# Optimization experiments

Measured on AMD Instinct MI355X. Metric: run time of the kernel, lower is better.

Reference implementation:

```python
import jax, jax.numpy as jnp
import numpy as np

PI = 3.141592653  # same constant as the torch source
M = 4
MIN_LAMBDA = 5.0
MAX_LAMBDA = 1500.0
IT = 1  # first forward call


def setup_inputs() -> dict:
    key = jax.random.key(0)
    k1, k2, k3 = jax.random.split(key, 3)
    N, D, C = 512, 512, 100000
    x = jax.random.normal(k1, (N, D), dtype=jnp.float32)
    target = jax.random.randint(k2, (N,), 0, C, dtype=jnp.int64)
    weight = jax.random.normal(k3, (D, C), dtype=jnp.float32)
    return {"x": x, "target": target, "weight": weight}


def reference(x, target, weight):
    # normalize weight columns (dim=0), as in F.normalize(w, p=2, dim=0)
    w = weight / jnp.linalg.norm(weight, axis=0, keepdims=True)
    w_norm = jnp.linalg.norm(w, axis=0, keepdims=True)          # [1, C] (~1)
    x_norm = jnp.linalg.norm(x, axis=1, keepdims=True)          # [N, 1]

    cos_theta = x @ w                                           # [N, C]
    cos_theta = jnp.clip(cos_theta / x_norm / w_norm, -1.0, 1.0)

    rows = jnp.arange(x.shape[0])
    c_t = cos_theta[rows, target]                               # [N]
    # m=4 multi-angle: cos(4t) = 8c^4 - 8c^2 + 1
    cos_m_theta = 8.0 * c_t ** 4 - 8.0 * c_t ** 2 + 1.0
    theta = jnp.arccos(c_t)
    k = jnp.floor(M * theta / PI)
    sign = 1.0 - 2.0 * (k % 2.0)                                # (-1)^k for integer-valued float k
    phi_t = sign * cos_m_theta - 2.0 * k

    cur_lambda = max(MIN_LAMBDA, MAX_LAMBDA / (1.0 + 0.1 * IT))
    addition = (phi_t - c_t) * x_norm[:, 0] / (1.0 + cur_lambda)

    out = cos_theta * x_norm                                    # [N, C]
    out = out.at[rows, target].add(addition)
    return out
```

## Files before the change

### kernel.cpp

```cpp
#include <hip/hip_runtime.h>
#include <hip/hip_bf16.h>

typedef __attribute__((ext_vector_type(4))) float f32x4;
typedef __attribute__((ext_vector_type(8))) short s16x8;

#define NR 512
#define KD 512
#define CC 100000
#define BN 32
#define LDSK 40

static __device__ __forceinline__ unsigned short f2bf(float f) {
    union { float f; unsigned u; } v; v.f = f;
    unsigned r = v.u + 0x7FFFu + ((v.u >> 16) & 1u);
    return (unsigned short)(r >> 16);
}

__global__ __launch_bounds__(256) void prep_kernel(const float* __restrict__ x,
                                                   float* __restrict__ xn,
                                                   unsigned short* __restrict__ xb) {
    const int row = blockIdx.x;
    const int t = threadIdx.x;
    const float* xr = x + row * KD;
    float v0 = xr[t];
    float v1 = xr[t + 256];
    float ss = v0 * v0 + v1 * v1;
    #pragma unroll
    for (int off = 32; off > 0; off >>= 1) ss += __shfl_down(ss, off, 64);
    __shared__ float sred[4];
    if ((t & 63) == 0) sred[t >> 6] = ss;
    __syncthreads();
    if (t == 0) xn[row] = sqrtf(sred[0] + sred[1] + sred[2] + sred[3]);
    xb[row * KD + t]       = f2bf(v0);
    xb[row * KD + t + 256] = f2bf(v1);
}

__global__ __launch_bounds__(256, 3) void gemm_kernel(const float* __restrict__ w,
                                                      const unsigned short* __restrict__ xb,
                                                      const float* __restrict__ xn,
                                                      float* __restrict__ out) {
    __shared__ unsigned short ldsB[BN * LDSK];
    __shared__ float sPart[8][BN];
    __shared__ float sInv[BN];

    const int t    = threadIdx.x;
    const int lane = t & 63;
    const int wv   = t >> 6;
    const int c0   = blockIdx.x * BN;
    const int cL   = t & 31;
    const int kq   = t >> 5;

    f32x4 acc[8][2];
    #pragma unroll
    for (int i = 0; i < 8; ++i) {
        acc[i][0] = {0.f, 0.f, 0.f, 0.f};
        acc[i][1] = {0.f, 0.f, 0.f, 0.f};
    }

    float ss = 0.0f;
    const int rowbase = wv * 128;
    const int arow = lane & 15;
    const int akq  = lane >> 4;

    const float* wp0 = w + (size_t)(kq * 4) * CC + c0 + cL;
    float bc0 = wp0[0];
    float bc1 = wp0[(size_t)CC];
    float bc2 = wp0[(size_t)2 * CC];
    float bc3 = wp0[(size_t)3 * CC];

    const unsigned short* abase = xb + (rowbase + arow) * KD + akq * 8;

    #pragma unroll 1
    for (int it = 0; it < 16; ++it) {
        const int kk = it * 32;

        s16x8 af[8];
        #pragma unroll
        for (int rt = 0; rt < 8; ++rt)
            af[rt] = *(const s16x8*)(abase + rt * 16 * KD + kk);

        float bn0 = 0.f, bn1 = 0.f, bn2 = 0.f, bn3 = 0.f;
        if (it < 15) {
            const float* wp = w + (size_t)(kk + 32 + kq * 4) * CC + c0 + cL;
            bn0 = wp[0];
            bn1 = wp[(size_t)CC];
            bn2 = wp[(size_t)2 * CC];
            bn3 = wp[(size_t)3 * CC];
        }

        ss += bc0 * bc0 + bc1 * bc1 + bc2 * bc2 + bc3 * bc3;
        ushort4 pk;
        pk.x = f2bf(bc0);
        pk.y = f2bf(bc1);
        pk.z = f2bf(bc2);
        pk.w = f2bf(bc3);

        __syncthreads();
        *(ushort4*)&ldsB[cL * LDSK + kq * 4] = pk;
        __syncthreads();

        const s16x8 bf0 = *(const s16x8*)&ldsB[(0 * 16 + arow) * LDSK + akq * 8];
        const s16x8 bf1 = *(const s16x8*)&ldsB[(1 * 16 + arow) * LDSK + akq * 8];

        #pragma unroll
        for (int rt = 0; rt < 8; ++rt) {
            acc[rt][0] = __builtin_amdgcn_mfma_f32_16x16x32_bf16(af[rt], bf0, acc[rt][0], 0, 0, 0);
            acc[rt][1] = __builtin_amdgcn_mfma_f32_16x16x32_bf16(af[rt], bf1, acc[rt][1], 0, 0, 0);
        }
        bc0 = bn0; bc1 = bn1; bc2 = bn2; bc3 = bn3;
    }

    sPart[kq][cL] = ss;
    __syncthreads();
    if (t < BN) {
        float tot = 0.f;
        #pragma unroll
        for (int i = 0; i < 8; ++i) tot += sPart[i][t];
        sInv[t] = 1.0f / sqrtf(tot);
    }
    __syncthreads();

    #pragma unroll
    for (int rt = 0; rt < 8; ++rt) {
        const int rbase = rowbase + rt * 16 + akq * 4;
        const f32x4 xnv = *(const f32x4*)(xn + rbase);
        #pragma unroll
        for (int ct = 0; ct < 2; ++ct) {
            const float inv = sInv[ct * 16 + arow];
            float* op = out + (size_t)rbase * CC + c0 + ct * 16 + arow;
            #pragma unroll
            for (int r = 0; r < 4; ++r) {
                float cv = acc[rt][ct][r] * inv / xnv[r];
                cv = fminf(1.0f, fmaxf(-1.0f, cv));
                op[(size_t)r * CC] = cv * xnv[r];
            }
        }
    }
}

__global__ __launch_bounds__(512) void fixup_kernel(const int* __restrict__ target,
                                                    const float* __restrict__ xn,
                                                    float* __restrict__ out) {
    const int i = threadIdx.x;
    const int tg = target[i];
    const float xni = xn[i];
    float* p = out + (size_t)i * CC + tg;
    const float val = *p;
    float c = val / xni;
    c = fminf(1.0f, fmaxf(-1.0f, c));
    const float c2 = c * c;
    const float cosm = 8.0f * c2 * c2 - 8.0f * c2 + 1.0f;
    const float theta = acosf(c);
    const float kf = floorf(4.0f * theta / 3.141592653f);
    const float sign = (((int)kf) & 1) ? -1.0f : 1.0f;
    const float phi = sign * cosm - 2.0f * kf;
    const float lam = 1500.0f / 1.1f;
    const float add = (phi - c) * xni / (1.0f + lam);
    *p = val + add;
}

extern "C" void kernel_launch(void* const* d_in, const int* in_sizes, int n_in,
                              void* d_out, int out_size, void* d_ws, size_t ws_size,
                              hipStream_t stream) {
    const float* x      = (const float*)d_in[0];
    const int*   target = (const int*)d_in[1];
    const float* w      = (const float*)d_in[2];
    float* out = (float*)d_out;

    float* xn = (float*)d_ws;
    unsigned short* xb = (unsigned short*)((char*)d_ws + 2048);

    prep_kernel<<<NR, 256, 0, stream>>>(x, xn, xb);
    gemm_kernel<<<CC / BN, 256, 0, stream>>>(w, xb, xn, out);
    fixup_kernel<<<1, 512, 0, stream>>>(target, xn, out);
}
```

Baseline: 522.0 us.

## Restructure GEMM tile to 64 columns with double-buffered LDS and deep weight prefetch

Widens the column tile to 64 and splits the rows across two blocks per column group, so each wave computes a 64x64 output tile. Weight loads are prefetched four stages ahead in registers, and the bf16 tile is double-buffered in LDS so each stage needs one barrier instead of two. It also raises MFMA priority, simplifies the clamp to avoid a divide, and writes the output with nontemporal stores. The cost is that each weight column is read by two blocks and each thread holds more live registers, which can lower occupancy.

Measured after the change: 566.7 us. 8.6% more time.

```diff
diff --git a/kernel.cpp b/kernel.cpp
--- a/kernel.cpp
+++ b/kernel.cpp
@@ -1,5 +1,4 @@
 #include <hip/hip_runtime.h>
-#include <hip/hip_bf16.h>
 
 typedef __attribute__((ext_vector_type(4))) float f32x4;
 typedef __attribute__((ext_vector_type(8))) short s16x8;
@@ -7,8 +6,9 @@
 #define NR 512
 #define KD 512
 #define CC 100000
-#define BN 32
+#define BN 64
 #define LDSK 40
+#define NSTG 16
 
 static __device__ __forceinline__ unsigned short f2bf(float f) {
     union { float f; unsigned u; } v; v.f = f;
@@ -35,104 +35,142 @@
     xb[row * KD + t + 256] = f2bf(v1);
 }
 
+#define CONVERT_STAGE(BUF, S)                                                        \
+  do {                                                                               \
+    ss += S[0]*S[0] + S[1]*S[1] + S[2]*S[2] + S[3]*S[3]                              \
+        + S[4]*S[4] + S[5]*S[5] + S[6]*S[6] + S[7]*S[7];                             \
+    ushort4 p0_, p1_;                                                                \
+    p0_.x = f2bf(S[0]); p0_.y = f2bf(S[1]); p0_.z = f2bf(S[2]); p0_.w = f2bf(S[3]);  \
+    p1_.x = f2bf(S[4]); p1_.y = f2bf(S[5]); p1_.z = f2bf(S[6]); p1_.w = f2bf(S[7]);  \
+    *(ushort4*)&ldsB[BUF][cL * LDSK + kg * 8]     = p0_;                             \
+    *(ushort4*)&ldsB[BUF][cL * LDSK + kg * 8 + 4] = p1_;                             \
+  } while (0)
+
 __global__ __launch_bounds__(256, 3) void gemm_kernel(const float* __restrict__ w,
                                                       const unsigned short* __restrict__ xb,
                                                       const float* __restrict__ xn,
                                                       float* __restrict__ out) {
-    __shared__ unsigned short ldsB[BN * LDSK];
-    __shared__ float sPart[8][BN];
+    __shared__ __align__(16) unsigned short ldsB[2][BN * LDSK];
+    __shared__ float sPart[4][BN];
     __shared__ float sInv[BN];
 
     const int t    = threadIdx.x;
     const int lane = t & 63;
     const int wv   = t >> 6;
-    const int c0   = blockIdx.x * BN;
-    const int cL   = t & 31;
-    const int kq   = t >> 5;
-
-    f32x4 acc[8][2];
-    #pragma unroll
-    for (int i = 0; i < 8; ++i) {
-        acc[i][0] = {0.f, 0.f, 0.f, 0.f};
-        acc[i][1] = {0.f, 0.f, 0.f, 0.f};
-    }
-
-    float ss = 0.0f;
-    const int rowbase = wv * 128;
+    const int ci   = blockIdx.x >> 1;
+    const int half = blockIdx.x & 1;
+    const int c0   = ci * BN;
+
+    const int cL = lane;
+    const int kg = wv;
+    int cg = c0 + cL;
+    if (cg > CC - 1) cg = CC - 1;
+    const float* wcol = w + cg;
+
+    const int rowbase = half * 256 + wv * 64;
     const int arow = lane & 15;
     const int akq  = lane >> 4;
-
-    const float* wp0 = w + (size_t)(kq * 4) * CC + c0 + cL;
-    float bc0 = wp0[0];
-    float bc1 = wp0[(size_t)CC];
-    float bc2 = wp0[(size_t)2 * CC];
-    float bc3 = wp0[(size_t)3 * CC];
-
-    const unsigned short* abase = xb + (rowbase + arow) * KD + akq * 8;
-
-    #pragma unroll 1
-    for (int it = 0; it < 16; ++it) {
-        const int kk = it * 32;
-
-        s16x8 af[8];
-        #pragma unroll
-        for (int rt = 0; rt < 8; ++rt)
-            af[rt] = *(const s16x8*)(abase + rt * 16 * KD + kk);
-
-        float bn0 = 0.f, bn1 = 0.f, bn2 = 0.f, bn3 = 0.f;
-        if (it < 15) {
-            const float* wp = w + (size_t)(kk + 32 + kq * 4) * CC + c0 + cL;
-            bn0 = wp[0];
-            bn1 = wp[(size_t)CC];
-            bn2 = wp[(size_t)2 * CC];
-            bn3 = wp[(size_t)3 * CC];
-        }
-
-        ss += bc0 * bc0 + bc1 * bc1 + bc2 * bc2 + bc3 * bc3;
-        ushort4 pk;
-        pk.x = f2bf(bc0);
-        pk.y = f2bf(bc1);
-        pk.z = f2bf(bc2);
-        pk.w = f2bf(bc3);
-
-        __syncthreads();
-        *(ushort4*)&ldsB[cL * LDSK + kq * 4] = pk;
-        __syncthreads();
-
-        const s16x8 bf0 = *(const s16x8*)&ldsB[(0 * 16 + arow) * LDSK + akq * 8];
-        const s16x8 bf1 = *(const s16x8*)&ldsB[(1 * 16 + arow) * LDSK + akq * 8];
-
-        #pragma unroll
-        for (int rt = 0; rt < 8; ++rt) {
-            acc[rt][0] = __builtin_amdgcn_mfma_f32_16x16x32_bf16(af[rt], bf0, acc[rt][0], 0, 0, 0);
-            acc[rt][1] = __builtin_amdgcn_mfma_f32_16x16x32_bf16(af[rt], bf1, acc[rt][1], 0, 0, 0);
-        }
-        bc0 = bn0; bc1 = bn1; bc2 = bn2; bc3 = bn3;
+    const unsigned short* abase = xb + (size_t)(rowbase + arow) * KD + akq * 8;
+
+    f32x4 acc[4][4];
+    #pragma unroll
+    for (int i = 0; i < 4; ++i)
+        #pragma unroll
+        for (int j = 0; j < 4; ++j)
+            acc[i][j] = {0.f, 0.f, 0.f, 0.f};
+
+    float ss = 0.f;
+
+    float s0[8], b0[8], b1[8], b2[8];
+    #pragma unroll
+    for (int r = 0; r < 8; ++r) s0[r] = wcol[(size_t)(kg * 8 + r) * CC];
+    s16x8 af[4];
+    #pragma unroll
+    for (int rt = 0; rt < 4; ++rt) af[rt] = *(const s16x8*)(abase + rt * 16 * KD);
+    #pragma unroll
+    for (int r = 0; r < 8; ++r) b0[r] = wcol[(size_t)(32 + kg * 8 + r) * CC];
+    #pragma unroll
+    for (int r = 0; r < 8; ++r) b1[r] = wcol[(size_t)(64 + kg * 8 + r) * CC];
+    #pragma unroll
+    for (int r = 0; r < 8; ++r) b2[r] = wcol[(size_t)(96 + kg * 8 + r) * CC];
+
+    CONVERT_STAGE(0, s0);
+    asm volatile("s_waitcnt lgkmcnt(0)" ::: "memory");
+    __builtin_amdgcn_s_barrier();
+
+    #pragma unroll
+    for (int i = 0; i < NSTG; ++i) {
+        s16x8 bf[4];
+        #pragma unroll
+        for (int ct = 0; ct < 4; ++ct)
+            bf[ct] = *(const s16x8*)&ldsB[i & 1][(ct * 16 + arow) * LDSK + akq * 8];
+
+        float bn[8];
+        if (i + 4 < NSTG) {
+            #pragma unroll
+            for (int r = 0; r < 8; ++r)
+                bn[r] = wcol[(size_t)((i + 4) * 32 + kg * 8 + r) * CC];
+        } else {
+            #pragma unroll
+            for (int r = 0; r < 8; ++r) bn[r] = 0.f;
+        }
+
+        s16x8 afn[4];
+        if (i + 1 < NSTG) {
+            #pragma unroll
+            for (int rt = 0; rt < 4; ++rt)
+                afn[rt] = *(const s16x8*)(abase + rt * 16 * KD + (i + 1) * 32);
+        } else {
+            #pragma unroll
+            for (int rt = 0; rt < 4; ++rt) afn[rt] = af[rt];
+        }
+
+        if (i + 1 < NSTG) {
+            CONVERT_STAGE((i + 1) & 1, b0);
+        }
+
+        asm volatile("s_waitcnt lgkmcnt(0)" ::: "memory");
+        __builtin_amdgcn_s_barrier();
+
+        __builtin_amdgcn_s_setprio(1);
+        #pragma unroll
+        for (int rt = 0; rt < 4; ++rt)
+            #pragma unroll
+            for (int ct = 0; ct < 4; ++ct)
+                acc[rt][ct] = __builtin_amdgcn_mfma_f32_16x16x32_bf16(af[rt], bf[ct], acc[rt][ct], 0, 0, 0);
+        __builtin_amdgcn_s_setprio(0);
+
+        #pragma unroll
+        for (int r = 0; r < 8; ++r) { b0[r] = b1[r]; b1[r] = b2[r]; b2[r] = bn[r]; }
+        #pragma unroll
+        for (int rt = 0; rt < 4; ++rt) af[rt] = afn[rt];
     }
 
-    sPart[kq][cL] = ss;
+    sPart[kg][cL] = ss;
     __syncthreads();
     if (t < BN) {
-        float tot = 0.f;
-        #pragma unroll
-        for (int i = 0; i < 8; ++i) tot += sPart[i][t];
+        const float tot = sPart[0][t] + sPart[1][t] + sPart[2][t] + sPart[3][t];
         sInv[t] = 1.0f / sqrtf(tot);
     }
     __syncthreads();
 
     #pragma unroll
-    for (int rt = 0; rt < 8; ++rt) {
+    for (int rt = 0; rt < 4; ++rt) {
         const int rbase = rowbase + rt * 16 + akq * 4;
         const f32x4 xnv = *(const f32x4*)(xn + rbase);
         #pragma unroll
-        for (int ct = 0; ct < 2; ++ct) {
-            const float inv = sInv[ct * 16 + arow];
-            float* op = out + (size_t)rbase * CC + c0 + ct * 16 + arow;
-            #pragma unroll
-            for (int r = 0; r < 4; ++r) {
-                float cv = acc[rt][ct][r] * inv / xnv[r];
-                cv = fminf(1.0f, fmaxf(-1.0f, cv));
-                op[(size_t)r * CC] = cv * xnv[r];
+        for (int ct = 0; ct < 4; ++ct) {
+            const int col = c0 + ct * 16 + arow;
+            if (col < CC) {
+                const float inv = sInv[ct * 16 + arow];
+                float* op = out + (size_t)rbase * CC + col;
+                #pragma unroll
+                for (int r = 0; r < 4; ++r) {
+                    float cv = acc[rt][ct][r] * inv;
+                    const float xr = xnv[r];
+                    cv = fminf(xr, fmaxf(-xr, cv));
+                    __builtin_nontemporal_store(cv, op + (size_t)r * CC);
+                }
             }
         }
     }
@@ -171,6 +209,7 @@
     unsigned short* xb = (unsigned short*)((char*)d_ws + 2048);
 
     prep_kernel<<<NR, 256, 0, stream>>>(x, xn, xb);
-    gemm_kernel<<<CC / BN, 256, 0, stream>>>(w, xb, xn, out);
+    const int nblk = ((CC + BN - 1) / BN) * 2;
+    gemm_kernel<<<nblk, 256, 0, stream>>>(w, xb, xn, out);
     fixup_kernel<<<1, 512, 0, stream>>>(target, xn, out);
 }
```

## Deepen weight prefetch pipeline with double-buffered LDS and single barrier

Applied to the files above, without the earlier changes.

Weight loads for the GEMM are now issued four k-stages ahead through a register queue, and the B tile is double-buffered in LDS so each iteration needs one barrier instead of two. The main loop is fully unrolled, and MFMA issue is given higher wave priority with s_setprio. The epilogue clamps the raw accumulator against ±xnorm directly, removing a division and a multiply per output. The aim is to hide global load latency in a memory-bound kernel, at the cost of more registers at 3 blocks per CU and a larger unrolled body.

Measured after the change: 521.2 us. About the same (-0.2%).

```diff
diff --git a/kernel.cpp b/kernel.cpp
--- a/kernel.cpp
+++ b/kernel.cpp
@@ -1,5 +1,4 @@
 #include <hip/hip_runtime.h>
-#include <hip/hip_bf16.h>
 
 typedef __attribute__((ext_vector_type(4))) float f32x4;
 typedef __attribute__((ext_vector_type(8))) short s16x8;
@@ -9,6 +8,7 @@
 #define CC 100000
 #define BN 32
 #define LDSK 40
+#define NSTG 16
 
 static __device__ __forceinline__ unsigned short f2bf(float f) {
     union { float f; unsigned u; } v; v.f = f;
@@ -35,11 +35,19 @@
     xb[row * KD + t + 256] = f2bf(v1);
 }
 
+#define CONVERT_STAGE(BUF, S)                                                        \
+  do {                                                                               \
+    ss += S[0]*S[0] + S[1]*S[1] + S[2]*S[2] + S[3]*S[3];                             \
+    ushort4 pk_;                                                                     \
+    pk_.x = f2bf(S[0]); pk_.y = f2bf(S[1]); pk_.z = f2bf(S[2]); pk_.w = f2bf(S[3]);  \
+    *(ushort4*)&ldsB[BUF][cL * LDSK + kq * 4] = pk_;                                 \
+  } while (0)
+
 __global__ __launch_bounds__(256, 3) void gemm_kernel(const float* __restrict__ w,
                                                       const unsigned short* __restrict__ xb,
                                                       const float* __restrict__ xn,
                                                       float* __restrict__ out) {
-    __shared__ unsigned short ldsB[BN * LDSK];
+    __shared__ __align__(16) unsigned short ldsB[2][BN * LDSK];
     __shared__ float sPart[8][BN];
     __shared__ float sInv[BN];
 
@@ -47,8 +55,15 @@
     const int lane = t & 63;
     const int wv   = t >> 6;
     const int c0   = blockIdx.x * BN;
-    const int cL   = t & 31;
-    const int kq   = t >> 5;
+
+    const int cL = t & 31;
+    const int kq = t >> 5;
+    const float* wcol = w + c0 + cL;
+
+    const int rowbase = wv * 128;
+    const int arow = lane & 15;
+    const int akq  = lane >> 4;
+    const unsigned short* abase = xb + (size_t)(rowbase + arow) * KD + akq * 8;
 
     f32x4 acc[8][2];
     #pragma unroll
@@ -57,57 +72,59 @@
         acc[i][1] = {0.f, 0.f, 0.f, 0.f};
     }
 
-    float ss = 0.0f;
-    const int rowbase = wv * 128;
-    const int arow = lane & 15;
-    const int akq  = lane >> 4;
+    float ss = 0.f;
 
-    const float* wp0 = w + (size_t)(kq * 4) * CC + c0 + cL;
-    float bc0 = wp0[0];
-    float bc1 = wp0[(size_t)CC];
-    float bc2 = wp0[(size_t)2 * CC];
-    float bc3 = wp0[(size_t)3 * CC];
+    float s0[4], b0[4], b1[4], b2[4];
+    #pragma unroll
+    for (int r = 0; r < 4; ++r) s0[r] = wcol[(size_t)(kq * 4 + r) * CC];
+    #pragma unroll
+    for (int r = 0; r < 4; ++r) b0[r] = wcol[(size_t)(32 + kq * 4 + r) * CC];
+    #pragma unroll
+    for (int r = 0; r < 4; ++r) b1[r] = wcol[(size_t)(64 + kq * 4 + r) * CC];
+    #pragma unroll
+    for (int r = 0; r < 4; ++r) b2[r] = wcol[(size_t)(96 + kq * 4 + r) * CC];
 
-    const unsigned short* abase = xb + (rowbase + arow) * KD + akq * 8;
+    CONVERT_STAGE(0, s0);
+    asm volatile("s_waitcnt lgkmcnt(0)" ::: "memory");
+    __builtin_amdgcn_s_barrier();
 
-    #pragma unroll 1
-    for (int it = 0; it < 16; ++it) {
-        const int kk = it * 32;
-
+    #pragma unroll
+    for (int i = 0; i < NSTG; ++i) {
         s16x8 af[8];
         #pragma unroll
         for (int rt = 0; rt < 8; ++rt)
-            af[rt] = *(const s16x8*)(abase + rt * 16 * KD + kk);
+            af[rt] = *(const s16x8*)(abase + rt * 16 * KD + i * 32);
 
-        float bn0 = 0.f, bn1 = 0.f, bn2 = 0.f, bn3 = 0.f;
-        if (it < 15) {
-            const float* wp = w + (size_t)(kk + 32 + kq * 4) * CC + c0 + cL;
-            bn0 = wp[0];
-            bn1 = wp[(size_t)CC];
-            bn2 = wp[(size_t)2 * CC];
-            bn3 = wp[(size_t)3 * CC];
+        const s16x8 bf0 = *(const s16x8*)&ldsB[i & 1][arow * LDSK + akq * 8];
+        const s16x8 bf1 = *(const s16x8*)&ldsB[i & 1][(16 + arow) * LDSK + akq * 8];
+
+        float bn[4];
+        if (i + 4 < NSTG) {
+            #pragma unroll
+            for (int r = 0; r < 4; ++r)
+                bn[r] = wcol[(size_t)((i + 4) * 32 + kq * 4 + r) * CC];
+        } else {
+            #pragma unroll
+            for (int r = 0; r < 4; ++r) bn[r] = 0.f;
         }
 
-        ss += bc0 * bc0 + bc1 * bc1 + bc2 * bc2 + bc3 * bc3;
-        ushort4 pk;
-        pk.x = f2bf(bc0);
-        pk.y = f2bf(bc1);
-        pk.z = f2bf(bc2);
-        pk.w = f2bf(bc3);
+        if (i + 1 < NSTG) {
+            CONVERT_STAGE((i + 1) & 1, b0);
+        }
 
-        __syncthreads();
-        *(ushort4*)&ldsB[cL * LDSK + kq * 4] = pk;
-        __syncthreads();
+        asm volatile("s_waitcnt lgkmcnt(0)" ::: "memory");
+        __builtin_amdgcn_s_barrier();
 
-        const s16x8 bf0 = *(const s16x8*)&ldsB[(0 * 16 + arow) * LDSK + akq * 8];
-        const s16x8 bf1 = *(const s16x8*)&ldsB[(1 * 16 + arow) * LDSK + akq * 8];
-
+        __builtin_amdgcn_s_setprio(1);
         #pragma unroll
         for (int rt = 0; rt < 8; ++rt) {
             acc[rt][0] = __builtin_amdgcn_mfma_f32_16x16x32_bf16(af[rt], bf0, acc[rt][0], 0, 0, 0);
             acc[rt][1] = __builtin_amdgcn_mfma_f32_16x16x32_bf16(af[rt], bf1, acc[rt][1], 0, 0, 0);
         }
-        bc0 = bn0; bc1 = bn1; bc2 = bn2; bc3 = bn3;
+        __builtin_amdgcn_s_setprio(0);
+
+        #pragma unroll
+        for (int r = 0; r < 4; ++r) { b0[r] = b1[r]; b1[r] = b2[r]; b2[r] = bn[r]; }
     }
 
     sPart[kq][cL] = ss;
@@ -130,9 +147,10 @@
             float* op = out + (size_t)rbase * CC + c0 + ct * 16 + arow;
             #pragma unroll
             for (int r = 0; r < 4; ++r) {
-                float cv = acc[rt][ct][r] * inv / xnv[r];
-                cv = fminf(1.0f, fmaxf(-1.0f, cv));
-                op[(size_t)r * CC] = cv * xnv[r];
+                float cv = acc[rt][ct][r] * inv;
+                const float xr = xnv[r];
+                cv = fminf(xr, fmaxf(-xr, cv));
+                op[(size_t)r * CC] = cv;
             }
         }
     }
```
